# Optimization experiments

Hardware: AMD Instinct MI355X
Metric: run time of the kernel (lower is better)

## Reference

```python
import jax, jax.numpy as jnp
import numpy as np

N_NODES = 50000
IN_DIM = 64
OUT_DIM = 128
N_EDGES = 800000


def setup_inputs() -> dict:
    key = jax.random.key(0)
    k1, k2, k3, k4, k5 = jax.random.split(key, 5)
    x = jax.random.normal(k1, (N_NODES, IN_DIM), dtype=jnp.float32)
    edge_index = jax.random.randint(k2, (2, N_EDGES), 0, N_NODES, dtype=jnp.int64)
    # PyG SAGEConv params: lin_l (neighbor path, with bias), lin_r (root path, no bias)
    s = 1.0 / np.sqrt(IN_DIM)
    W_l = jax.random.uniform(k3, (OUT_DIM, IN_DIM), dtype=jnp.float32, minval=-s, maxval=s)
    b_l = jax.random.uniform(k4, (OUT_DIM,), dtype=jnp.float32, minval=-s, maxval=s)
    W_r = jax.random.uniform(k5, (OUT_DIM, IN_DIM), dtype=jnp.float32, minval=-s, maxval=s)
    return {"x": x, "edge_index": edge_index, "W_l": W_l, "b_l": b_l, "W_r": W_r}


def reference(x, edge_index, W_l, b_l, W_r):
    # Single-layer GraphSAGE (PyG SAGEConv, mean aggregation).
    # BasicGNN applies no activation after the last (only) layer.
    src = edge_index[0]  # message sources
    dst = edge_index[1]  # aggregation targets
    n = x.shape[0]
    # gather neighbor features and mean-aggregate per destination node
    summed = jax.ops.segment_sum(x[src], dst, num_segments=n)          # [N, IN_DIM]
    cnt = jax.ops.segment_sum(jnp.ones_like(src, dtype=x.dtype), dst, num_segments=n)
    mean = summed / jnp.clip(cnt, 1.0)[:, None]
    # out = lin_l(mean_neighbors) + lin_r(x)
    out = mean @ W_l.T + b_l + x @ W_r.T                               # [N, OUT_DIM]
    return out
```

## Files before the change

### kernel.cpp

```cpp
#include <hip/hip_runtime.h>

#define N_NODES 50000
#define IN_DIM 64
#define OUT_DIM 128
#define N_EDGES 800000

#define NBLK 128
#define EPB (N_EDGES / NBLK)
#define NBUCK 391
#define WLDS 136
#define FIXSCALE 1048576.0f
#define INVFIX (1.0f / 1048576.0f)

typedef __attribute__((ext_vector_type(8))) short bf16x8;
typedef __attribute__((ext_vector_type(4))) float f32x4;

__device__ __forceinline__ unsigned short f2bf(float f) {
    unsigned u = __float_as_uint(f);
    unsigned r = u + 0x7FFFu + ((u >> 16) & 1u);
    return (unsigned short)(r >> 16);
}

__global__ __launch_bounds__(256) void bucket_count_cvt(const int* __restrict__ ei,
                                                        const float* __restrict__ x,
                                                        const float* __restrict__ Wl,
                                                        const float* __restrict__ Wr,
                                                        int* __restrict__ cnt_mat,
                                                        unsigned short* __restrict__ xh,
                                                        unsigned short* __restrict__ w2h)
{
    __shared__ int h[NBUCK];
    int t = threadIdx.x, blk = blockIdx.x;
    for (int i = t; i < NBUCK; i += 256) h[i] = 0;
    __syncthreads();
    int s = blk * EPB;
    for (int i = s + t; i < s + EPB; i += 256)
        atomicAdd(&h[ei[N_EDGES + i] >> 7], 1);
    for (int i = t; i < 6250; i += 256) {
        int gi = blk * 6250 + i;
        float4 v = ((const float4*)x)[gi];
        ushort4 o;
        o.x = f2bf(v.x); o.y = f2bf(v.y); o.z = f2bf(v.z); o.w = f2bf(v.w);
        ((ushort4*)xh)[gi] = o;
    }
    if (t < 64) {
        w2h[blk * 128 + t]      = f2bf(Wr[blk * 64 + t]);
        w2h[blk * 128 + 64 + t] = f2bf(Wl[blk * 64 + t]);
    }
    __syncthreads();
    for (int b = t; b < NBUCK; b += 256) cnt_mat[b * NBLK + blk] = h[b];
}

__global__ __launch_bounds__(256) void rowscan(int* __restrict__ cnt_mat)
{
    __shared__ int tot[NBUCK];
    __shared__ int bst[NBUCK];
    int t = threadIdx.x, lane = t & 63, wid = t >> 6;
    for (int b = t; b < NBUCK; b += 256) {
        const int4* row = (const int4*)(cnt_mat + b * NBLK);
        int sum = 0;
#pragma unroll 8
        for (int i = 0; i < NBLK / 4; ++i) { int4 v = row[i]; sum += v.x + v.y + v.z + v.w; }
        tot[b] = sum;
    }
    __syncthreads();
    if (wid == 0) {
        int carry = 0;
        for (int base = 0; base < NBUCK; base += 64) {
            int i = base + lane;
            int v = (i < NBUCK) ? tot[i] : 0;
            int incl = v;
#pragma unroll
            for (int d = 1; d < 64; d <<= 1) {
                int u = __shfl_up(incl, d, 64);
                if (lane >= d) incl += u;
            }
            if (i < NBUCK) bst[i] = carry + incl - v;
            carry += __shfl(incl, 63, 64);
        }
    }
    __syncthreads();
    int b = blockIdx.x * 4 + wid;
    if (b >= NBUCK) return;
    int base = bst[b];
#pragma unroll
    for (int c = 0; c < 2; ++c) {
        int idx = c * 64 + lane;
        int cv = cnt_mat[b * NBLK + idx];
        int ic = cv;
#pragma unroll
        for (int d = 1; d < 64; d <<= 1) {
            int u = __shfl_up(ic, d, 64);
            if (lane >= d) ic += u;
        }
        cnt_mat[b * NBLK + idx] = base + ic - cv;
        base += __shfl(ic, 63, 64);
    }
}

__global__ __launch_bounds__(256) void bucket_place(const int* __restrict__ ei,
                                                    const int* __restrict__ cnt_scan,
                                                    unsigned* __restrict__ ebuf)
{
    __shared__ int cur[NBUCK];
    int t = threadIdx.x, blk = blockIdx.x;
    for (int b = t; b < NBUCK; b += 256) cur[b] = cnt_scan[b * NBLK + blk];
    __syncthreads();
    int s = blk * EPB;
    for (int i = s + t; i < s + EPB; i += 256) {
        int src = ei[i], dst = ei[N_EDGES + i];
        int slot = atomicAdd(&cur[dst >> 7], 1);
        ebuf[slot] = (unsigned)src | ((unsigned)(dst & 127) << 16);
    }
}

__global__ __launch_bounds__(1024) void gather_mfma(const unsigned short* __restrict__ xh,
                                                    const int* __restrict__ cnt_scan,
                                                    const unsigned* __restrict__ ebuf,
                                                    const unsigned short* __restrict__ w2h,
                                                    const float* __restrict__ bl,
                                                    float* __restrict__ out)
{
    __shared__ int acc[128 * 64];
    __shared__ unsigned short wlds[128 * WLDS];
    __shared__ int dcnt[128];
    __shared__ int range_s[2];
    int t = threadIdx.x, b = blockIdx.x;
    int lane = t & 63, w = t >> 6;

#pragma unroll
    for (int c = 0; c < 2; ++c) {
        int idx = c * 1024 + t;
        int o = idx >> 4, kc = idx & 15;
        bf16x8 v = *(const bf16x8*)(w2h + o * 128 + kc * 8);
        *(bf16x8*)(&wlds[o * WLDS + kc * 8]) = v;
    }
    if (t == 0) {
        range_s[0] = cnt_scan[b * NBLK];
        range_s[1] = (b < NBUCK - 1) ? cnt_scan[(b + 1) * NBLK] : N_EDGES;
    }
#pragma unroll
    for (int i = 0; i < 8; ++i) acc[i * 1024 + t] = 0;
    if (t < 128) dcnt[t] = 0;
    __syncthreads();

    int bs = range_s[0], be = range_s[1];

    for (int e = bs + t; e < be; e += 1024)
        atomicAdd(&dcnt[(ebuf[e] >> 16) & 127], 1);

    for (int e0 = bs + w * 64; e0 < be; e0 += 1024) {
        int m = be - e0; if (m > 64) m = 64;
        unsigned pv = (lane < m) ? ebuf[e0 + lane] : 0u;
        for (int k = 0; k < m; k += 8) {
            unsigned p[8]; int fx[8];
#pragma unroll
            for (int u = 0; u < 8; ++u) p[u] = __shfl(pv, k + u, 64);
#pragma unroll
            for (int u = 0; u < 8; ++u) {
                unsigned short hv = xh[(size_t)(p[u] & 0xFFFFu) * IN_DIM + lane];
                float f = __uint_as_float((unsigned)hv << 16);
                fx[u] = __float2int_rn(f * FIXSCALE);
            }
#pragma unroll
            for (int u = 0; u < 8; ++u)
                if (k + u < m)
                    atomicAdd(&acc[((p[u] >> 16) & 127) * 64 + lane], fx[u]);
        }
    }
    __syncthreads();

    int s_strip = w & 7, hf = w >> 3;
    int nbase = b * 128 + s_strip * 16;
    if (nbase >= N_NODES) return;
    int row = lane & 15, q = lane >> 4;
    int nn = nbase + row;
    size_t nrow = (size_t)((nn < N_NODES) ? nn : (N_NODES - 1));

    bf16x8 a[4];
    a[0] = *(const bf16x8*)(xh + nrow * IN_DIM + q * 8);
    a[1] = *(const bf16x8*)(xh + nrow * IN_DIM + q * 8 + 32);

    int in_node = s_strip * 16 + row;
    int deg = dcnt[in_node];
    float sc = deg ? INVFIX / (float)deg : 0.0f;
    bf16x8 a2, a3;
#pragma unroll
    for (int j = 0; j < 8; ++j) {
        float f0 = (float)acc[in_node * 64 + q * 8 + j] * sc;
        float f1 = (float)acc[in_node * 64 + 32 + q * 8 + j] * sc;
        a2[j] = (short)f2bf(f0);
        a3[j] = (short)f2bf(f1);
    }
    a[2] = a2; a[3] = a3;

    f32x4 accf[4];
#pragma unroll
    for (int jj = 0; jj < 4; ++jj) accf[jj] = (f32x4){0.f, 0.f, 0.f, 0.f};

#pragma unroll
    for (int jj = 0; jj < 4; ++jj) {
        int ot = hf * 4 + jj;
        const unsigned short* wb = &wlds[(ot * 16 + row) * WLDS + q * 8];
#pragma unroll
        for (int s = 0; s < 4; ++s) {
            bf16x8 bfrag = *(const bf16x8*)(wb + s * 32);
            accf[jj] = __builtin_amdgcn_mfma_f32_16x16x32_bf16(a[s], bfrag, accf[jj], 0, 0, 0);
        }
    }

#pragma unroll
    for (int jj = 0; jj < 4; ++jj) {
        int ot = hf * 4 + jj;
        float bias = bl[ot * 16 + row];
#pragma unroll
        for (int r = 0; r < 4; ++r) {
            int n = nbase + q * 4 + r;
            if (n < N_NODES)
                out[(size_t)n * OUT_DIM + ot * 16 + row] = accf[jj][r] + bias;
        }
    }
}

extern "C" void kernel_launch(void* const* d_in, const int* in_sizes, int n_in,
                              void* d_out, int out_size, void* d_ws, size_t ws_size,
                              hipStream_t stream) {
    const float* x  = (const float*)d_in[0];
    const int*   ei = (const int*)d_in[1];
    const float* Wl = (const float*)d_in[2];
    const float* bl = (const float*)d_in[3];
    const float* Wr = (const float*)d_in[4];
    float* out = (float*)d_out;

    int*            cnt_mat = (int*)d_ws;
    unsigned*       ebuf    = (unsigned*)(cnt_mat + NBUCK * NBLK);
    unsigned short* xh      = (unsigned short*)(ebuf + N_EDGES);
    unsigned short* w2h     = xh + (size_t)N_NODES * IN_DIM;

    bucket_count_cvt<<<NBLK, 256, 0, stream>>>(ei, x, Wl, Wr, cnt_mat, xh, w2h);
    rowscan<<<(NBUCK + 3) / 4, 256, 0, stream>>>(cnt_mat);
    bucket_place<<<NBLK, 256, 0, stream>>>(ei, cnt_mat, ebuf);
    gather_mfma<<<NBUCK, 1024, 0, stream>>>(xh, cnt_mat, ebuf, w2h, bl, out);
}
```

Measured before the change: 79.14 us.

## Fuse four-kernel pipeline into one persistent kernel with grid barriers

Replaces the count, scan, place and gather kernels with a single kernel of 196 blocks that coordinates phases through a software grid barrier in global memory. Buckets grow to 256 nodes, the LDS accumulator uses an XOR swizzle to reduce bank conflicts, and the gather loop unrolls 16 edges per step. Each wave now computes all 8 output tiles for its 16 nodes. This removes launch gaps and intermediate kernel boundaries. The cost is grid-barrier spin overhead and a co-residency requirement: all 196 blocks of 1024 threads with large LDS must be resident at once, or the barrier deadlocks.

```diff
diff --git a/kernel.cpp b/kernel.cpp
--- a/kernel.cpp
+++ b/kernel.cpp
@@ -5,9 +5,8 @@
 #define OUT_DIM 128
 #define N_EDGES 800000
 
-#define NBLK 128
-#define EPB (N_EDGES / NBLK)
-#define NBUCK 391
+#define NB 196
+#define ES 4082
 #define WLDS 136
 #define FIXSCALE 1048576.0f
 #define INVFIX (1.0f / 1048576.0f)
@@ -21,159 +20,170 @@
     return (unsigned short)(r >> 16);
 }
 
-__global__ __launch_bounds__(256) void bucket_count_cvt(const int* __restrict__ ei,
-                                                        const float* __restrict__ x,
-                                                        const float* __restrict__ Wl,
-                                                        const float* __restrict__ Wr,
-                                                        int* __restrict__ cnt_mat,
-                                                        unsigned short* __restrict__ xh,
-                                                        unsigned short* __restrict__ w2h)
+__device__ __forceinline__ int SW(int nd, int f) { return (nd << 6) + (f ^ ((nd & 7) << 3)); }
+
+__device__ __forceinline__ void gbar(int* cnt, int* gen) {
+    __syncthreads();
+    if (threadIdx.x == 0) {
+        __threadfence();
+        int g = __hip_atomic_load(gen, __ATOMIC_RELAXED, __HIP_MEMORY_SCOPE_AGENT);
+        int a = __hip_atomic_fetch_add(cnt, 1, __ATOMIC_ACQ_REL, __HIP_MEMORY_SCOPE_AGENT);
+        if (a == NB - 1) {
+            __hip_atomic_store(cnt, 0, __ATOMIC_RELAXED, __HIP_MEMORY_SCOPE_AGENT);
+            __hip_atomic_fetch_add(gen, 1, __ATOMIC_RELEASE, __HIP_MEMORY_SCOPE_AGENT);
+        } else {
+            while (__hip_atomic_load(gen, __ATOMIC_ACQUIRE, __HIP_MEMORY_SCOPE_AGENT) == g)
+                __builtin_amdgcn_s_sleep(2);
+        }
+        __threadfence();
+    }
+    __syncthreads();
+}
+
+__global__ __launch_bounds__(1024, 4) void sage_mega(
+    const float* __restrict__ x, const int* __restrict__ ei,
+    const float* __restrict__ Wl, const float* __restrict__ bl,
+    const float* __restrict__ Wr,
+    int* __restrict__ bar,
+    int* __restrict__ cnt_mat,
+    int* __restrict__ tot,
+    unsigned* __restrict__ ebuf,
+    unsigned short* __restrict__ xh,
+    float* __restrict__ out)
 {
-    __shared__ int h[NBUCK];
-    int t = threadIdx.x, blk = blockIdx.x;
-    for (int i = t; i < NBUCK; i += 256) h[i] = 0;
-    __syncthreads();
-    int s = blk * EPB;
-    for (int i = s + t; i < s + EPB; i += 256)
-        atomicAdd(&h[ei[N_EDGES + i] >> 7], 1);
-    for (int i = t; i < 6250; i += 256) {
-        int gi = blk * 6250 + i;
-        float4 v = ((const float4*)x)[gi];
-        ushort4 o;
-        o.x = f2bf(v.x); o.y = f2bf(v.y); o.z = f2bf(v.z); o.w = f2bf(v.w);
-        ((ushort4*)xh)[gi] = o;
-    }
+    __shared__ int acc[256 * 64];
+    __shared__ unsigned short wlds[128 * WLDS];
+    __shared__ int histcur[NB];
+    __shared__ int rowpref[NB];
+    __shared__ int dcnt[256];
+    __shared__ float bls[128];
+    __shared__ int bsbe[2];
+
+    const int t = threadIdx.x, b = blockIdx.x;
+    const int lane = t & 63, w = t >> 6;
+    const int* dsti = ei + N_EDGES;
+    int* cnt_b = bar + 0;
+    int* gen_b = bar + 1;
+
+    for (int idx = t; idx < 128 * 32; idx += 1024) {
+        int o = idx >> 5, c4 = idx & 31;
+        const float* srcw = (c4 < 16) ? (Wr + o * 64 + c4 * 4)
+                                      : (Wl + o * 64 + (c4 - 16) * 4);
+        float4 v = *(const float4*)srcw;
+        ushort4 h4;
+        h4.x = f2bf(v.x); h4.y = f2bf(v.y); h4.z = f2bf(v.z); h4.w = f2bf(v.w);
+        *(ushort4*)(&wlds[o * WLDS + c4 * 4]) = h4;
+    }
+    if (t < 128) bls[t] = bl[t];
+
+    const int r0 = b * 256;
+    for (int idx = t; idx < 256 * 16; idx += 1024) {
+        int row = idx >> 4, c4 = idx & 15;
+        int g = r0 + row;
+        if (g < N_NODES) {
+            float4 v = ((const float4*)x)[g * 16 + c4];
+            ushort4 h4;
+            h4.x = f2bf(v.x); h4.y = f2bf(v.y); h4.z = f2bf(v.z); h4.w = f2bf(v.w);
+            ((ushort4*)xh)[g * 16 + c4] = h4;
+        }
+    }
+
+    for (int i = t; i < NB; i += 1024) histcur[i] = 0;
+    __syncthreads();
+    const int es = b * ES;
+    const int ee = min(es + ES, N_EDGES);
+    for (int e = es + t; e < ee; e += 1024)
+        atomicAdd(&histcur[dsti[e] >> 8], 1);
+    __syncthreads();
+    for (int j = t; j < NB; j += 1024) cnt_mat[j * NB + b] = histcur[j];
+
+    gbar(cnt_b, gen_b);
+
     if (t < 64) {
-        w2h[blk * 128 + t]      = f2bf(Wr[blk * 64 + t]);
-        w2h[blk * 128 + 64 + t] = f2bf(Wl[blk * 64 + t]);
-    }
-    __syncthreads();
-    for (int b = t; b < NBUCK; b += 256) cnt_mat[b * NBLK + blk] = h[b];
-}
-
-__global__ __launch_bounds__(256) void rowscan(int* __restrict__ cnt_mat)
-{
-    __shared__ int tot[NBUCK];
-    __shared__ int bst[NBUCK];
-    int t = threadIdx.x, lane = t & 63, wid = t >> 6;
-    for (int b = t; b < NBUCK; b += 256) {
-        const int4* row = (const int4*)(cnt_mat + b * NBLK);
-        int sum = 0;
-#pragma unroll 8
-        for (int i = 0; i < NBLK / 4; ++i) { int4 v = row[i]; sum += v.x + v.y + v.z + v.w; }
-        tot[b] = sum;
-    }
-    __syncthreads();
-    if (wid == 0) {
         int carry = 0;
-        for (int base = 0; base < NBUCK; base += 64) {
-            int i = base + lane;
-            int v = (i < NBUCK) ? tot[i] : 0;
+#pragma unroll
+        for (int c = 0; c < 4; ++c) {
+            int i = c * 64 + t;
+            int v = (i < NB) ? cnt_mat[b * NB + i] : 0;
             int incl = v;
 #pragma unroll
             for (int d = 1; d < 64; d <<= 1) {
                 int u = __shfl_up(incl, d, 64);
-                if (lane >= d) incl += u;
-            }
-            if (i < NBUCK) bst[i] = carry + incl - v;
+                if (t >= d) incl += u;
+            }
+            if (i < NB) rowpref[i] = carry + incl - v;
             carry += __shfl(incl, 63, 64);
         }
-    }
-    __syncthreads();
-    int b = blockIdx.x * 4 + wid;
-    if (b >= NBUCK) return;
-    int base = bst[b];
-#pragma unroll
-    for (int c = 0; c < 2; ++c) {
-        int idx = c * 64 + lane;
-        int cv = cnt_mat[b * NBLK + idx];
-        int ic = cv;
-#pragma unroll
-        for (int d = 1; d < 64; d <<= 1) {
-            int u = __shfl_up(ic, d, 64);
-            if (lane >= d) ic += u;
-        }
-        cnt_mat[b * NBLK + idx] = base + ic - cv;
-        base += __shfl(ic, 63, 64);
-    }
-}
-
-__global__ __launch_bounds__(256) void bucket_place(const int* __restrict__ ei,
-                                                    const int* __restrict__ cnt_scan,
-                                                    unsigned* __restrict__ ebuf)
-{
-    __shared__ int cur[NBUCK];
-    int t = threadIdx.x, blk = blockIdx.x;
-    for (int b = t; b < NBUCK; b += 256) cur[b] = cnt_scan[b * NBLK + blk];
-    __syncthreads();
-    int s = blk * EPB;
-    for (int i = s + t; i < s + EPB; i += 256) {
-        int src = ei[i], dst = ei[N_EDGES + i];
-        int slot = atomicAdd(&cur[dst >> 7], 1);
-        ebuf[slot] = (unsigned)src | ((unsigned)(dst & 127) << 16);
-    }
-}
-
-__global__ __launch_bounds__(1024) void gather_mfma(const unsigned short* __restrict__ xh,
-                                                    const int* __restrict__ cnt_scan,
-                                                    const unsigned* __restrict__ ebuf,
-                                                    const unsigned short* __restrict__ w2h,
-                                                    const float* __restrict__ bl,
-                                                    float* __restrict__ out)
-{
-    __shared__ int acc[128 * 64];
-    __shared__ unsigned short wlds[128 * WLDS];
-    __shared__ int dcnt[128];
-    __shared__ int range_s[2];
-    int t = threadIdx.x, b = blockIdx.x;
-    int lane = t & 63, w = t >> 6;
-
-#pragma unroll
-    for (int c = 0; c < 2; ++c) {
-        int idx = c * 1024 + t;
-        int o = idx >> 4, kc = idx & 15;
-        bf16x8 v = *(const bf16x8*)(w2h + o * 128 + kc * 8);
-        *(bf16x8*)(&wlds[o * WLDS + kc * 8]) = v;
-    }
-    if (t == 0) {
-        range_s[0] = cnt_scan[b * NBLK];
-        range_s[1] = (b < NBUCK - 1) ? cnt_scan[(b + 1) * NBLK] : N_EDGES;
-    }
-#pragma unroll
-    for (int i = 0; i < 8; ++i) acc[i * 1024 + t] = 0;
-    if (t < 128) dcnt[t] = 0;
-    __syncthreads();
-
-    int bs = range_s[0], be = range_s[1];
+        if (t == 0) tot[b] = carry;
+    }
+
+    gbar(cnt_b, gen_b);
+
+    if (t < 64) {
+        int carry = 0;
+#pragma unroll
+        for (int c = 0; c < 4; ++c) {
+            int i = c * 64 + t;
+            int v = (i < NB) ? tot[i] : 0;
+            int incl = v;
+#pragma unroll
+            for (int d = 1; d < 64; d <<= 1) {
+                int u = __shfl_up(incl, d, 64);
+                if (t >= d) incl += u;
+            }
+            if (i == b) bsbe[0] = carry + incl - v;
+            carry += __shfl(incl, 63, 64);
+        }
+    }
+    __syncthreads();
+    for (int j = t; j < NB; j += 1024) cnt_mat[b * NB + j] = bsbe[0] + rowpref[j];
+    if (t == 0) bsbe[1] = bsbe[0] + tot[b];
+
+    gbar(cnt_b, gen_b);
+
+    for (int j = t; j < NB; j += 1024) histcur[j] = cnt_mat[j * NB + b];
+#pragma unroll
+    for (int i = 0; i < 16; ++i) acc[i * 1024 + t] = 0;
+    if (t < 256) dcnt[t] = 0;
+    __syncthreads();
+    for (int e = es + t; e < ee; e += 1024) {
+        int src = ei[e], dst = dsti[e];
+        int pos = atomicAdd(&histcur[dst >> 8], 1);
+        ebuf[pos] = (unsigned)src | ((unsigned)(dst & 255) << 16);
+    }
+
+    gbar(cnt_b, gen_b);
+
+    const int bs = bsbe[0], be = bsbe[1];
 
     for (int e = bs + t; e < be; e += 1024)
-        atomicAdd(&dcnt[(ebuf[e] >> 16) & 127], 1);
+        atomicAdd(&dcnt[(ebuf[e] >> 16) & 255], 1);
 
     for (int e0 = bs + w * 64; e0 < be; e0 += 1024) {
         int m = be - e0; if (m > 64) m = 64;
         unsigned pv = (lane < m) ? ebuf[e0 + lane] : 0u;
-        for (int k = 0; k < m; k += 8) {
-            unsigned p[8]; int fx[8];
-#pragma unroll
-            for (int u = 0; u < 8; ++u) p[u] = __shfl(pv, k + u, 64);
-#pragma unroll
-            for (int u = 0; u < 8; ++u) {
+        for (int k = 0; k < m; k += 16) {
+            unsigned p[16]; int fx[16];
+#pragma unroll
+            for (int u = 0; u < 16; ++u) p[u] = __shfl(pv, k + u, 64);
+#pragma unroll
+            for (int u = 0; u < 16; ++u) {
                 unsigned short hv = xh[(size_t)(p[u] & 0xFFFFu) * IN_DIM + lane];
-                float f = __uint_as_float((unsigned)hv << 16);
-                fx[u] = __float2int_rn(f * FIXSCALE);
-            }
-#pragma unroll
-            for (int u = 0; u < 8; ++u)
-                if (k + u < m)
-                    atomicAdd(&acc[((p[u] >> 16) & 127) * 64 + lane], fx[u]);
-        }
-    }
-    __syncthreads();
-
-    int s_strip = w & 7, hf = w >> 3;
-    int nbase = b * 128 + s_strip * 16;
-    if (nbase >= N_NODES) return;
-    int row = lane & 15, q = lane >> 4;
+                fx[u] = __float2int_rn(__uint_as_float((unsigned)hv << 16) * FIXSCALE);
+            }
+#pragma unroll
+            for (int u = 0; u < 16; ++u) {
+                if (k + u < m) {
+                    int nd = (p[u] >> 16) & 255;
+                    atomicAdd(&acc[SW(nd, lane)], fx[u]);
+                }
+            }
+        }
+    }
+    __syncthreads();
+
+    const int nbase = b * 256 + w * 16;
+    const int row = lane & 15, q = lane >> 4;
     int nn = nbase + row;
     size_t nrow = (size_t)((nn < N_NODES) ? nn : (N_NODES - 1));
 
@@ -181,43 +191,39 @@
     a[0] = *(const bf16x8*)(xh + nrow * IN_DIM + q * 8);
     a[1] = *(const bf16x8*)(xh + nrow * IN_DIM + q * 8 + 32);
 
-    int in_node = s_strip * 16 + row;
+    const int in_node = w * 16 + row;
     int deg = dcnt[in_node];
     float sc = deg ? INVFIX / (float)deg : 0.0f;
     bf16x8 a2, a3;
 #pragma unroll
     for (int j = 0; j < 8; ++j) {
-        float f0 = (float)acc[in_node * 64 + q * 8 + j] * sc;
-        float f1 = (float)acc[in_node * 64 + 32 + q * 8 + j] * sc;
-        a2[j] = (short)f2bf(f0);
-        a3[j] = (short)f2bf(f1);
+        a2[j] = (short)f2bf((float)acc[SW(in_node, q * 8 + j)] * sc);
+        a3[j] = (short)f2bf((float)acc[SW(in_node, 32 + q * 8 + j)] * sc);
     }
     a[2] = a2; a[3] = a3;
 
-    f32x4 accf[4];
-#pragma unroll
-    for (int jj = 0; jj < 4; ++jj) accf[jj] = (f32x4){0.f, 0.f, 0.f, 0.f};
-
-#pragma unroll
-    for (int jj = 0; jj < 4; ++jj) {
-        int ot = hf * 4 + jj;
+    f32x4 accf[8];
+#pragma unroll
+    for (int ot = 0; ot < 8; ++ot) accf[ot] = (f32x4){0.f, 0.f, 0.f, 0.f};
+
+#pragma unroll
+    for (int ot = 0; ot < 8; ++ot) {
         const unsigned short* wb = &wlds[(ot * 16 + row) * WLDS + q * 8];
 #pragma unroll
         for (int s = 0; s < 4; ++s) {
             bf16x8 bfrag = *(const bf16x8*)(wb + s * 32);
-            accf[jj] = __builtin_amdgcn_mfma_f32_16x16x32_bf16(a[s], bfrag, accf[jj], 0, 0, 0);
-        }
-    }
-
-#pragma unroll
-    for (int jj = 0; jj < 4; ++jj) {
-        int ot = hf * 4 + jj;
-        float bias = bl[ot * 16 + row];
+            accf[ot] = __builtin_amdgcn_mfma_f32_16x16x32_bf16(a[s], bfrag, accf[ot], 0, 0, 0);
+        }
+    }
+
+#pragma unroll
+    for (int ot = 0; ot < 8; ++ot) {
+        float bias = bls[ot * 16 + row];
 #pragma unroll
         for (int r = 0; r < 4; ++r) {
             int n = nbase + q * 4 + r;
             if (n < N_NODES)
-                out[(size_t)n * OUT_DIM + ot * 16 + row] = accf[jj][r] + bias;
+                out[(size_t)n * OUT_DIM + ot * 16 + row] = accf[ot][r] + bias;
         }
     }
 }
@@ -232,13 +238,13 @@
     const float* Wr = (const float*)d_in[4];
     float* out = (float*)d_out;
 
-    int*            cnt_mat = (int*)d_ws;
-    unsigned*       ebuf    = (unsigned*)(cnt_mat + NBUCK * NBLK);
+    int*            bar     = (int*)d_ws;
+    int*            cnt_mat = bar + 8;
+    int*            tot     = cnt_mat + NB * NB;
+    unsigned*       ebuf    = (unsigned*)(tot + NB);
     unsigned short* xh      = (unsigned short*)(ebuf + N_EDGES);
-    unsigned short* w2h     = xh + (size_t)N_NODES * IN_DIM;
-
-    bucket_count_cvt<<<NBLK, 256, 0, stream>>>(ei, x, Wl, Wr, cnt_mat, xh, w2h);
-    rowscan<<<(NBUCK + 3) / 4, 256, 0, stream>>>(cnt_mat);
-    bucket_place<<<NBLK, 256, 0, stream>>>(ei, cnt_mat, ebuf);
-    gather_mfma<<<NBUCK, 1024, 0, stream>>>(xh, cnt_mat, ebuf, w2h, bl, out);
-}
+
+    hipMemsetAsync(bar, 0, 8 * sizeof(int), stream);
+    sage_mega<<<NB, 1024, 0, stream>>>(x, ei, Wl, bl, Wr,
+                                       bar, cnt_mat, tot, ebuf, xh, out);
+}
```

Measured after the change: 179.2 us. +126.5%, slower.
